# Performance work log

Measured on AMD Instinct MI355X. Metric: run time of the kernel, lower is better.

## Reference

```python
import jax, jax.numpy as jnp
import numpy as np

B, L, H, NH, NB = 8, 200, 128, 4, 2
HD = H // NH
ITEM_NUM, TIME_SPAN = 50000, 256
PAD = -2.0**32 + 1.0


def setup_inputs() -> dict:
    key = jax.random.key(0)
    ks = jax.random.split(key, 32)
    def g(i, shape, s=0.02):
        return jax.random.normal(ks[i], shape, jnp.float32) * s
    item_emb = g(0, (ITEM_NUM + 1, H)).at[0].set(0.0)  # padding_idx=0
    return dict(
        user_ids=jax.random.randint(ks[1], (B,), 0, 1000),
        log_seqs=jax.random.randint(ks[2], (B, L), 0, ITEM_NUM),
        time_matrices=jax.random.randint(ks[3], (B, L, L), 0, TIME_SPAN + 1),
        pos_seqs=jax.random.randint(ks[4], (B, L), 0, ITEM_NUM + 1),
        neg_seqs=jax.random.randint(ks[5], (B, L), 0, ITEM_NUM + 1),
        item_emb=item_emb,
        pos_K_emb=g(6, (L, H)), pos_V_emb=g(7, (L, H)),
        time_K_emb=g(8, (TIME_SPAN + 1, H)), time_V_emb=g(9, (TIME_SPAN + 1, H)),
        attn_ln_g=jnp.ones((NB, H)), attn_ln_b=jnp.zeros((NB, H)),
        Wq=g(10, (NB, H, H)), bq=jnp.zeros((NB, H)),
        Wk=g(11, (NB, H, H)), bk=jnp.zeros((NB, H)),
        Wv=g(12, (NB, H, H)), bv=jnp.zeros((NB, H)),
        fwd_ln_g=jnp.ones((NB, H)), fwd_ln_b=jnp.zeros((NB, H)),
        W1=g(13, (NB, H, H)), b1=jnp.zeros((NB, H)),
        W2=g(14, (NB, H, H)), b2=jnp.zeros((NB, H)),
        last_ln_g=jnp.ones((H,)), last_ln_b=jnp.zeros((H,)),
    )


def _ln(x, g, b, eps=1e-8):
    m = x.mean(-1, keepdims=True)
    v = jnp.var(x, axis=-1, keepdims=True)
    return (x - m) / jnp.sqrt(v + eps) * g + b


def _heads(x):
    # [..., H] -> [NH, ..., HD]; matches torch.cat(torch.split(x, HD, -1), 0)
    y = x.reshape(x.shape[:-1] + (NH, HD))
    return jnp.moveaxis(y, -2, 0)


def reference(user_ids, log_seqs, time_matrices, pos_seqs, neg_seqs, item_emb,
              pos_K_emb, pos_V_emb, time_K_emb, time_V_emb,
              attn_ln_g, attn_ln_b, Wq, bq, Wk, bk, Wv, bv,
              fwd_ln_g, fwd_ln_b, W1, b1, W2, b2, last_ln_g, last_ln_b):
    # user_ids is unused in the original forward as well.
    tmask = log_seqs == 0                                  # [B,L] True = pad
    keep = (~tmask)[..., None].astype(jnp.float32)
    seqs = item_emb[log_seqs] * np.float32(np.sqrt(H))
    seqs = seqs * keep
    pKh = _heads(pos_K_emb)                                # [NH,L,HD]
    pVh = _heads(pos_V_emb)
    tKh = _heads(time_K_emb[time_matrices])                # [NH,B,L,L,HD]
    tVh = _heads(time_V_emb[time_matrices])
    causal = ~jnp.tril(jnp.ones((L, L), bool))             # True above diag -> masked
    bad = tmask[:, :, None] | causal[None]                 # [B,L,L]
    scale = np.float32(np.sqrt(HD))
    for i in range(NB):
        Qin = _ln(seqs, attn_ln_g[i], attn_ln_b[i])
        Qh = _heads(Qin @ Wq[i].T + bq[i])                 # [NH,B,L,HD]
        Kh = _heads(seqs @ Wk[i].T + bk[i])
        Vh = _heads(seqs @ Wv[i].T + bv[i])
        attn = (jnp.einsum('nbqd,nbkd->nbqk', Qh, Kh)
                + jnp.einsum('nbqd,nkd->nbqk', Qh, pKh)
                + jnp.einsum('nbqkd,nbqd->nbqk', tKh, Qh)) / scale
        attn = jnp.where(bad[None], PAD, attn)
        attn = jax.nn.softmax(attn, axis=-1)
        out = (jnp.einsum('nbqk,nbkd->nbqd', attn, Vh)
               + jnp.einsum('nbqk,nkd->nbqd', attn, pVh)
               + jnp.einsum('nbqk,nbqkd->nbqd', attn, tVh))
        out = jnp.moveaxis(out, 0, -2).reshape(seqs.shape)  # merge heads -> [B,L,H]
        seqs = Qin + out                                    # residual uses LN'd Q (as in source)
        seqs = _ln(seqs, fwd_ln_g[i], fwd_ln_b[i])
        ff = jax.nn.relu(seqs @ W1[i].T + b1[i]) @ W2[i].T + b2[i] + seqs
        seqs = ff * keep
    log_feats = _ln(seqs, last_ln_g, last_ln_b)
    pos_logits = (log_feats * item_emb[pos_seqs]).sum(-1)   # [B,L]
    neg_logits = (log_feats * item_emb[neg_seqs]).sum(-1)
    return pos_logits, neg_logits
```

## Files before the change

kernel.cpp:

```cpp
#include <hip/hip_runtime.h>
#include <hip/hip_bf16.h>

#define BB 8
#define LL 200
#define HH 128
#define NHEAD 4
#define HDIM 32
#define NBLK 2
#define BL (BB * LL)
#define NT 257
#define QT 8
#define NQT 25
#define SSP 208
#define KTP 66
#define ASP 36
#define BSP 66
#define FASP 20
#define RSP 132

static constexpr float SQRT_H    = 11.313708498984761f;
static constexpr float INV_SCALE = 0.17677669529663687f;
static constexpr float PADV      = -4294967295.0f;

__global__ void k_qkv_gemm(const float* __restrict__ seqs_in,
                           const int* __restrict__ log_seqs,
                           const float* __restrict__ item_emb,
                           const float* __restrict__ g, const float* __restrict__ bia,
                           const float* __restrict__ Wq, const float* __restrict__ bq,
                           const float* __restrict__ Wk, const float* __restrict__ bk,
                           const float* __restrict__ Wv, const float* __restrict__ bv,
                           const float* __restrict__ posK, const float* __restrict__ posV,
                           float* __restrict__ Qin, float* __restrict__ Q,
                           float* __restrict__ K, float* __restrict__ V) {
    int mt = blockIdx.x / 6, nt = blockIdx.x % 6;
    int matsel = nt >> 1;
    int jb = (nt & 1) * 64;
    int row0 = mt * 32;
    int tid = threadIdx.x;
    __shared__ float As[128 * ASP];
    __shared__ float Bs[128 * BSP];

    {
        int r = tid >> 3, seg = tid & 7;
        int row = row0 + r;
        float4 vv[4];
        if (seqs_in) {
            #pragma unroll
            for (int i = 0; i < 4; i++)
                vv[i] = *(const float4*)(seqs_in + (size_t)row * HH + seg * 16 + i * 4);
        } else {
            int idx = log_seqs[row];
            if (idx == 0) {
                #pragma unroll
                for (int i = 0; i < 4; i++) vv[i] = make_float4(0.f, 0.f, 0.f, 0.f);
            } else {
                #pragma unroll
                for (int i = 0; i < 4; i++) {
                    float4 e = *(const float4*)(item_emb + (size_t)idx * HH + seg * 16 + i * 4);
                    vv[i] = make_float4(e.x * SQRT_H, e.y * SQRT_H, e.z * SQRT_H, e.w * SQRT_H);
                }
            }
        }
        if (matsel == 0) {
            float s = 0.f, s2 = 0.f;
            #pragma unroll
            for (int i = 0; i < 4; i++) {
                s  += vv[i].x + vv[i].y + vv[i].z + vv[i].w;
                s2 += vv[i].x * vv[i].x + vv[i].y * vv[i].y + vv[i].z * vv[i].z + vv[i].w * vv[i].w;
            }
            #pragma unroll
            for (int off = 1; off < 8; off <<= 1) {
                s  += __shfl_xor(s, off);
                s2 += __shfl_xor(s2, off);
            }
            float mean = s * (1.f / HH);
            float var  = s2 * (1.f / HH) - mean * mean;
            float inv  = 1.f / sqrtf(var + 1e-8f);
            #pragma unroll
            for (int i = 0; i < 4; i++) {
                int k = seg * 16 + i * 4;
                float4 g4 = *(const float4*)(g + k);
                float4 b4 = *(const float4*)(bia + k);
                float4 y;
                y.x = (vv[i].x - mean) * inv * g4.x + b4.x;
                y.y = (vv[i].y - mean) * inv * g4.y + b4.y;
                y.z = (vv[i].z - mean) * inv * g4.z + b4.z;
                y.w = (vv[i].w - mean) * inv * g4.w + b4.w;
                As[(k + 0) * ASP + r] = y.x;
                As[(k + 1) * ASP + r] = y.y;
                As[(k + 2) * ASP + r] = y.z;
                As[(k + 3) * ASP + r] = y.w;
                if (nt == 0) *(float4*)(Qin + (size_t)row * HH + k) = y;
            }
        } else {
            #pragma unroll
            for (int i = 0; i < 4; i++) {
                int k = seg * 16 + i * 4;
                As[(k + 0) * ASP + r] = vv[i].x;
                As[(k + 1) * ASP + r] = vv[i].y;
                As[(k + 2) * ASP + r] = vv[i].z;
                As[(k + 3) * ASP + r] = vv[i].w;
            }
        }
    }
    {
        const float* W = (matsel == 0) ? Wq : (matsel == 1) ? Wk : Wv;
        int k4 = tid & 31, jj0 = tid >> 5;
        #pragma unroll
        for (int p = 0; p < 8; p++) {
            int jj = jj0 + p * 8;
            float4 w = *(const float4*)(W + (size_t)(jb + jj) * HH + k4 * 4);
            Bs[(k4 * 4 + 0) * BSP + jj] = w.x;
            Bs[(k4 * 4 + 1) * BSP + jj] = w.y;
            Bs[(k4 * 4 + 2) * BSP + jj] = w.z;
            Bs[(k4 * 4 + 3) * BSP + jj] = w.w;
        }
    }
    __syncthreads();

    int my = tid >> 5, jx = tid & 31;
    float a00=0,a01=0,a10=0,a11=0,a20=0,a21=0,a30=0,a31=0;
    #pragma unroll 4
    for (int k = 0; k < HH; k++) {
        float4 a = *(const float4*)&As[k * ASP + my * 4];
        float2 b = *(const float2*)&Bs[k * BSP + jx * 2];
        a00 += a.x * b.x; a01 += a.x * b.y;
        a10 += a.y * b.x; a11 += a.y * b.y;
        a20 += a.z * b.x; a21 += a.z * b.y;
        a30 += a.w * b.x; a31 += a.w * b.y;
    }
    float accs[4][2] = {{a00,a01},{a10,a11},{a20,a21},{a30,a31}};
    int col = jb + jx * 2;
    if (matsel == 0) {
        float2 bb = *(const float2*)(bq + col);
        #pragma unroll
        for (int r = 0; r < 4; r++) {
            int row = row0 + my * 4 + r;
            float2 o = make_float2((accs[r][0] + bb.x) * INV_SCALE,
                                   (accs[r][1] + bb.y) * INV_SCALE);
            *(float2*)(Q + (size_t)row * HH + col) = o;
        }
    } else if (matsel == 1) {
        float2 bb = *(const float2*)(bk + col);
        #pragma unroll
        for (int r = 0; r < 4; r++) {
            int row = row0 + my * 4 + r;
            int l = row % LL;
            float2 pk = *(const float2*)(posK + (size_t)l * HH + col);
            float2 o = make_float2(accs[r][0] + bb.x + pk.x, accs[r][1] + bb.y + pk.y);
            *(float2*)(K + (size_t)row * HH + col) = o;
        }
    } else {
        float2 bb = *(const float2*)(bv + col);
        #pragma unroll
        for (int r = 0; r < 4; r++) {
            int row = row0 + my * 4 + r;
            int l = row % LL;
            float2 pv = *(const float2*)(posV + (size_t)l * HH + col);
            float2 o = make_float2(accs[r][0] + bb.x + pv.x, accs[r][1] + bb.y + pv.y);
            *(float2*)(V + (size_t)row * HH + col) = o;
        }
    }
}

__global__ void k_attn(const float* __restrict__ Q, const float* __restrict__ K,
                       const float* __restrict__ V,
                       const float* __restrict__ timeK, const float* __restrict__ timeV,
                       const int* __restrict__ tm,
                       float* __restrict__ att) {
    int bn = blockIdx.x & 31;
    int b = bn >> 2, n = bn & 3;
    int qt = (NQT - 1) - (blockIdx.x >> 5);
    int q0 = qt * QT;
    int kmax = q0 + QT - 1;
    int tid = threadIdx.x;
    int wv = tid >> 6, ln = tid & 63;

    __shared__ float Qs[QT * HDIM];
    __shared__ float KstT[HDIM * KTP];
    __shared__ float DTW[QT * NT];
    __shared__ float Ssc[QT * SSP];
    __shared__ int   tmst[QT * LL];
    __shared__ float Ost[QT * HDIM];

    Ost[tid] = 0.f;
    if (tid < 64) {
        int qi = tid >> 3, d4 = tid & 7;
        *(float4*)(Qs + qi * HDIM + d4 * 4) =
            *(const float4*)(Q + ((size_t)(b * LL + q0 + qi)) * HH + n * HDIM + d4 * 4);
    }
    #pragma unroll
    for (int qi = 0; qi < QT; qi++)
        if (tid < LL)
            tmst[qi * LL + tid] = tm[((size_t)(b * LL + q0 + qi)) * LL + tid];
    __syncthreads();

    int k2 = tid & 31, qi_c = tid >> 5;

    for (int c = 0; c < 5; c++) {
        #pragma unroll
        for (int p = 0; p < 2; p++) {
            int idx = tid + p * 256;
            int r = idx >> 3, d4 = idx & 7;
            int tau = c * 64 + r;
            float4 w = make_float4(0.f, 0.f, 0.f, 0.f);
            if (tau < NT) w = *(const float4*)(timeK + (size_t)tau * HH + n * HDIM + d4 * 4);
            KstT[(d4 * 4 + 0) * KTP + r] = w.x;
            KstT[(d4 * 4 + 1) * KTP + r] = w.y;
            KstT[(d4 * 4 + 2) * KTP + r] = w.z;
            KstT[(d4 * 4 + 3) * KTP + r] = w.w;
        }
        __syncthreads();
        float a0 = 0.f, a1 = 0.f;
        #pragma unroll 4
        for (int d = 0; d < HDIM; d++) {
            float qv = Qs[qi_c * HDIM + d];
            float2 kv = *(const float2*)&KstT[d * KTP + k2 * 2];
            a0 += qv * kv.x; a1 += qv * kv.y;
        }
        int tau0 = c * 64 + k2 * 2;
        if (tau0 < NT)     DTW[qi_c * NT + tau0]     = a0;
        if (tau0 + 1 < NT) DTW[qi_c * NT + tau0 + 1] = a1;
        __syncthreads();
    }

    int nch = (kmax >> 6) + 1;
    for (int c = 0; c < nch; c++) {
        #pragma unroll
        for (int p = 0; p < 2; p++) {
            int idx = tid + p * 256;
            int r = idx >> 3, d4 = idx & 7;
            int k = c * 64 + r;
            float4 w = make_float4(0.f, 0.f, 0.f, 0.f);
            if (k < LL) w = *(const float4*)(K + ((size_t)(b * LL + k)) * HH + n * HDIM + d4 * 4);
            KstT[(d4 * 4 + 0) * KTP + r] = w.x;
            KstT[(d4 * 4 + 1) * KTP + r] = w.y;
            KstT[(d4 * 4 + 2) * KTP + r] = w.z;
            KstT[(d4 * 4 + 3) * KTP + r] = w.w;
        }
        __syncthreads();
        float a0 = 0.f, a1 = 0.f;
        #pragma unroll 4
        for (int d = 0; d < HDIM; d++) {
            float qv = Qs[qi_c * HDIM + d];
            float2 kv = *(const float2*)&KstT[d * KTP + k2 * 2];
            a0 += qv * kv.x; a1 += qv * kv.y;
        }
        int q = q0 + qi_c;
        int k0 = c * 64 + k2 * 2;
        if (k0 <= kmax)
            Ssc[qi_c * SSP + k0] = (k0 <= q) ? (a0 + DTW[qi_c * NT + tmst[qi_c * LL + k0]]) : PADV;
        if (k0 + 1 <= kmax)
            Ssc[qi_c * SSP + k0 + 1] = (k0 + 1 <= q) ? (a1 + DTW[qi_c * NT + tmst[qi_c * LL + k0 + 1]]) : PADV;
        __syncthreads();
    }

    for (int idx = tid; idx < QT * NT; idx += 256) DTW[idx] = 0.f;
    __syncthreads();

    for (int rr = 0; rr < 2; rr++) {
        int qi = wv + rr * 4;
        int q = q0 + qi;
        float sv[4];
        float m = PADV;
        #pragma unroll
        for (int jj = 0; jj < 4; jj++) {
            int k = ln + 64 * jj;
            sv[jj] = (k <= q) ? Ssc[qi * SSP + k] : PADV;
            m = fmaxf(m, sv[jj]);
        }
        for (int off = 32; off; off >>= 1) m = fmaxf(m, __shfl_xor(m, off));
        float sum = 0.f;
        #pragma unroll
        for (int jj = 0; jj < 4; jj++) {
            int k = ln + 64 * jj;
            sv[jj] = (k <= q) ? __expf(sv[jj] - m) : 0.f;
            sum += sv[jj];
        }
        for (int off = 32; off; off >>= 1) sum += __shfl_xor(sum, off);
        float inv = 1.f / sum;
        #pragma unroll
        for (int jj = 0; jj < 4; jj++) {
            int k = ln + 64 * jj;
            float p = sv[jj] * inv;
            if (k < SSP) Ssc[qi * SSP + k] = (k <= q) ? p : 0.f;
            if (k <= q) atomicAdd(&DTW[qi * NT + tmst[qi * LL + k]], p);
        }
    }
    __syncthreads();

    int d = tid & 31, kg = tid >> 5;
    float acc[QT] = {0,0,0,0,0,0,0,0};
    const float* vb = V + ((size_t)(b * LL)) * HH + n * HDIM + d;
    for (int k = kg; k <= kmax; k += 8) {
        float v = vb[(size_t)k * HH];
        #pragma unroll
        for (int qi = 0; qi < QT; qi++) acc[qi] += Ssc[qi * SSP + k] * v;
    }
    const float* tvb = timeV + n * HDIM + d;
    for (int t = kg; t < NT; t += 8) {
        float v = tvb[(size_t)t * HH];
        #pragma unroll
        for (int qi = 0; qi < QT; qi++) acc[qi] += DTW[qi * NT + t] * v;
    }
    #pragma unroll
    for (int qi = 0; qi < QT; qi++) atomicAdd(&Ost[qi * HDIM + d], acc[qi]);
    __syncthreads();
    {
        int qi = tid >> 5;
        att[((size_t)(b * LL + q0 + qi)) * HH + n * HDIM + d] = Ost[qi * HDIM + d];
    }
}

__global__ void k_ff1(const float* __restrict__ Qin, const float* __restrict__ att,
                      const float* __restrict__ g, const float* __restrict__ bia,
                      const float* __restrict__ W1, const float* __restrict__ b1,
                      float* __restrict__ h1) {
    int mt = blockIdx.x >> 1, nt = blockIdx.x & 1;
    int jb = nt * 64;
    int row0 = mt * 16;
    int tid = threadIdx.x;
    __shared__ float As[128 * FASP];
    __shared__ float Bs[128 * BSP];

    {
        int r = tid >> 4, seg = tid & 15;
        int row = row0 + r;
        float4 vv[2];
        #pragma unroll
        for (int i = 0; i < 2; i++) {
            int k = seg * 8 + i * 4;
            float4 q4 = *(const float4*)(Qin + (size_t)row * HH + k);
            float4 a4 = *(const float4*)(att + (size_t)row * HH + k);
            vv[i] = make_float4(q4.x + a4.x, q4.y + a4.y, q4.z + a4.z, q4.w + a4.w);
        }
        float s = 0.f, s2 = 0.f;
        #pragma unroll
        for (int i = 0; i < 2; i++) {
            s  += vv[i].x + vv[i].y + vv[i].z + vv[i].w;
            s2 += vv[i].x * vv[i].x + vv[i].y * vv[i].y + vv[i].z * vv[i].z + vv[i].w * vv[i].w;
        }
        #pragma unroll
        for (int off = 1; off < 16; off <<= 1) {
            s  += __shfl_xor(s, off);
            s2 += __shfl_xor(s2, off);
        }
        float mean = s * (1.f / HH);
        float var  = s2 * (1.f / HH) - mean * mean;
        float inv  = 1.f / sqrtf(var + 1e-8f);
        #pragma unroll
        for (int i = 0; i < 2; i++) {
            int k = seg * 8 + i * 4;
            float4 g4 = *(const float4*)(g + k);
            float4 b4 = *(const float4*)(bia + k);
            As[(k + 0) * FASP + r] = (vv[i].x - mean) * inv * g4.x + b4.x;
            As[(k + 1) * FASP + r] = (vv[i].y - mean) * inv * g4.y + b4.y;
            As[(k + 2) * FASP + r] = (vv[i].z - mean) * inv * g4.z + b4.z;
            As[(k + 3) * FASP + r] = (vv[i].w - mean) * inv * g4.w + b4.w;
        }
    }
    {
        int k4 = tid & 31, jj0 = tid >> 5;
        #pragma unroll
        for (int p = 0; p < 8; p++) {
            int jj = jj0 + p * 8;
            float4 w = *(const float4*)(W1 + (size_t)(jb + jj) * HH + k4 * 4);
            Bs[(k4 * 4 + 0) * BSP + jj] = w.x;
            Bs[(k4 * 4 + 1) * BSP + jj] = w.y;
            Bs[(k4 * 4 + 2) * BSP + jj] = w.z;
            Bs[(k4 * 4 + 3) * BSP + jj] = w.w;
        }
    }
    __syncthreads();

    int my = tid >> 5, jx = tid & 31;
    float a00 = 0, a01 = 0, a10 = 0, a11 = 0;
    #pragma unroll 4
    for (int k = 0; k < HH; k++) {
        float2 a = *(const float2*)&As[k * FASP + my * 2];
        float2 b = *(const float2*)&Bs[k * BSP + jx * 2];
        a00 += a.x * b.x; a01 += a.x * b.y;
        a10 += a.y * b.x; a11 += a.y * b.y;
    }
    int col = jb + jx * 2;
    float2 bb = *(const float2*)(b1 + col);
    {
        int row = row0 + my * 2;
        float2 o0 = make_float2(fmaxf(a00 + bb.x, 0.f), fmaxf(a01 + bb.y, 0.f));
        float2 o1 = make_float2(fmaxf(a10 + bb.x, 0.f), fmaxf(a11 + bb.y, 0.f));
        *(float2*)(h1 + (size_t)row * HH + col) = o0;
        *(float2*)(h1 + (size_t)(row + 1) * HH + col) = o1;
    }
}

__global__ void k_ff2(const float* __restrict__ h1,
                      const float* __restrict__ Qin, const float* __restrict__ att,
                      const float* __restrict__ g, const float* __restrict__ bia,
                      const float* __restrict__ W2, const float* __restrict__ b2,
                      const int* __restrict__ log_seqs,
                      float* __restrict__ out) {
    int mt = blockIdx.x >> 1, nt = blockIdx.x & 1;
    int jb = nt * 64;
    int row0 = mt * 16;
    int tid = threadIdx.x;
    __shared__ float As[128 * FASP];
    __shared__ float Bs[128 * BSP];
    __shared__ float Rs[16 * RSP];
    __shared__ float mu[16], rstd[16];

    {
        int r = tid >> 4, seg = tid & 15;
        int row = row0 + r;
        #pragma unroll
        for (int i = 0; i < 2; i++) {
            int k = seg * 8 + i * 4;
            float4 h4 = *(const float4*)(h1 + (size_t)row * HH + k);
            As[(k + 0) * FASP + r] = h4.x;
            As[(k + 1) * FASP + r] = h4.y;
            As[(k + 2) * FASP + r] = h4.z;
            As[(k + 3) * FASP + r] = h4.w;
        }
        float s = 0.f, s2 = 0.f;
        #pragma unroll
        for (int i = 0; i < 2; i++) {
            int k = seg * 8 + i * 4;
            float4 q4 = *(const float4*)(Qin + (size_t)row * HH + k);
            float4 a4 = *(const float4*)(att + (size_t)row * HH + k);
            float4 v = make_float4(q4.x + a4.x, q4.y + a4.y, q4.z + a4.z, q4.w + a4.w);
            *(float4*)(Rs + r * RSP + k) = v;
            s  += v.x + v.y + v.z + v.w;
            s2 += v.x * v.x + v.y * v.y + v.z * v.z + v.w * v.w;
        }
        #pragma unroll
        for (int off = 1; off < 16; off <<= 1) {
            s  += __shfl_xor(s, off);
            s2 += __shfl_xor(s2, off);
        }
        float mean = s * (1.f / HH);
        float var  = s2 * (1.f / HH) - mean * mean;
        if (seg == 0) { mu[r] = mean; rstd[r] = 1.f / sqrtf(var + 1e-8f); }
    }
    {
        int k4 = tid & 31, jj0 = tid >> 5;
        #pragma unroll
        for (int p = 0; p < 8; p++) {
            int jj = jj0 + p * 8;
            float4 w = *(const float4*)(W2 + (size_t)(jb + jj) * HH + k4 * 4);
            Bs[(k4 * 4 + 0) * BSP + jj] = w.x;
            Bs[(k4 * 4 + 1) * BSP + jj] = w.y;
            Bs[(k4 * 4 + 2) * BSP + jj] = w.z;
            Bs[(k4 * 4 + 3) * BSP + jj] = w.w;
        }
    }
    __syncthreads();

    int my = tid >> 5, jx = tid & 31;
    float a00 = 0, a01 = 0, a10 = 0, a11 = 0;
    #pragma unroll 4
    for (int k = 0; k < HH; k++) {
        float2 a = *(const float2*)&As[k * FASP + my * 2];
        float2 b = *(const float2*)&Bs[k * BSP + jx * 2];
        a00 += a.x * b.x; a01 += a.x * b.y;
        a10 += a.y * b.x; a11 += a.y * b.y;
    }
    int col = jb + jx * 2;
    float2 bb = *(const float2*)(b2 + col);
    float2 g2 = *(const float2*)(g + col);
    float2 lb = *(const float2*)(bia + col);
    float accs[2][2] = {{a00, a01}, {a10, a11}};
    #pragma unroll
    for (int r = 0; r < 2; r++) {
        int ri = my * 2 + r;
        int row = row0 + ri;
        float m = mu[ri], iv = rstd[ri];
        float2 R = *(const float2*)&Rs[ri * RSP + col];
        float y0 = (R.x - m) * iv * g2.x + lb.x;
        float y1 = (R.y - m) * iv * g2.y + lb.y;
        float2 o = make_float2(accs[r][0] + bb.x + y0, accs[r][1] + bb.y + y1);
        if (log_seqs[row] == 0) o = make_float2(0.f, 0.f);
        *(float2*)(out + (size_t)row * HH + col) = o;
    }
}

__global__ void k_lnlogits(const float* __restrict__ seqs,
                           const float* __restrict__ g, const float* __restrict__ bia,
                           const float* __restrict__ item_emb,
                           const int* __restrict__ pos, const int* __restrict__ neg,
                           float* __restrict__ out) {
    int row = blockIdx.x;
    int h = threadIdx.x;
    float v = seqs[(size_t)row * HH + h];
    float s = v, s2 = v * v;
    for (int off = 32; off; off >>= 1) {
        s  += __shfl_xor(s, off);
        s2 += __shfl_xor(s2, off);
    }
    __shared__ float r1[2], r2[2];
    if ((h & 63) == 0) { r1[h >> 6] = s; r2[h >> 6] = s2; }
    __syncthreads();
    float mean = (r1[0] + r1[1]) * (1.f / HH);
    float var  = (r2[0] + r2[1]) * (1.f / HH) - mean * mean;
    float inv = 1.f / sqrtf(var + 1e-8f);
    float f = (v - mean) * inv * g[h] + bia[h];

    int ip = pos[row], in_ = neg[row];
    float vp = f * item_emb[(size_t)ip * HH + h];
    float vn = f * item_emb[(size_t)in_ * HH + h];
    for (int off = 32; off; off >>= 1) {
        vp += __shfl_xor(vp, off);
        vn += __shfl_xor(vn, off);
    }
    __shared__ float rp[2], rn[2];
    if ((h & 63) == 0) { rp[h >> 6] = vp; rn[h >> 6] = vn; }
    __syncthreads();
    if (h == 0) {
        out[row]      = rp[0] + rp[1];
        out[BL + row] = rn[0] + rn[1];
    }
}

extern "C" void kernel_launch(void* const* d_in, const int* in_sizes, int n_in,
                              void* d_out, int out_size, void* d_ws, size_t ws_size,
                              hipStream_t stream) {
    const int* log_seqs   = (const int*)d_in[1];
    const int* tm         = (const int*)d_in[2];
    const int* pos_seqs   = (const int*)d_in[3];
    const int* neg_seqs   = (const int*)d_in[4];
    const float* item_emb = (const float*)d_in[5];
    const float* posK     = (const float*)d_in[6];
    const float* posV     = (const float*)d_in[7];
    const float* timeK    = (const float*)d_in[8];
    const float* timeV    = (const float*)d_in[9];
    const float* attn_g   = (const float*)d_in[10];
    const float* attn_b   = (const float*)d_in[11];
    const float* Wq       = (const float*)d_in[12];
    const float* bq       = (const float*)d_in[13];
    const float* Wk       = (const float*)d_in[14];
    const float* bk       = (const float*)d_in[15];
    const float* Wv       = (const float*)d_in[16];
    const float* bv       = (const float*)d_in[17];
    const float* fwd_g    = (const float*)d_in[18];
    const float* fwd_b    = (const float*)d_in[19];
    const float* W1       = (const float*)d_in[20];
    const float* b1       = (const float*)d_in[21];
    const float* W2       = (const float*)d_in[22];
    const float* b2       = (const float*)d_in[23];
    const float* last_g   = (const float*)d_in[24];
    const float* last_b   = (const float*)d_in[25];

    float* seqs = (float*)d_ws;
    float* Qin  = seqs + (size_t)BL * HH;
    float* Qb   = Qin  + (size_t)BL * HH;
    float* Kb   = Qb   + (size_t)BL * HH;
    float* Vb   = Kb   + (size_t)BL * HH;
    float* att  = Vb   + (size_t)BL * HH;
    float* h1   = att  + (size_t)BL * HH;

    for (int i = 0; i < NBLK; i++) {
        k_qkv_gemm<<<300, 256, 0, stream>>>(i == 0 ? nullptr : seqs, log_seqs, item_emb,
                                            attn_g + i * HH, attn_b + i * HH,
                                            Wq + (size_t)i * HH * HH, bq + i * HH,
                                            Wk + (size_t)i * HH * HH, bk + i * HH,
                                            Wv + (size_t)i * HH * HH, bv + i * HH,
                                            posK, posV, Qin, Qb, Kb, Vb);
        k_attn<<<NQT * 32, 256, 0, stream>>>(Qb, Kb, Vb, timeK, timeV, tm, att);
        k_ff1<<<200, 256, 0, stream>>>(Qin, att, fwd_g + i * HH, fwd_b + i * HH,
                                       W1 + (size_t)i * HH * HH, b1 + i * HH, h1);
        k_ff2<<<200, 256, 0, stream>>>(h1, Qin, att, fwd_g + i * HH, fwd_b + i * HH,
                                       W2 + (size_t)i * HH * HH, b2 + i * HH,
                                       log_seqs, seqs);
    }
    k_lnlogits<<<BL, HH, 0, stream>>>(seqs, last_g, last_b, item_emb,
                                      pos_seqs, neg_seqs, (float*)d_out);
}
```

Baseline: 241.0 us.

## Shrink GEMM output tiles and use row-major LDS dot-product layout

The QKV, FF1 and FF2 GEMMs now use 16-column output tiles, giving four times more blocks so more CUs stay busy on this small problem. Shared-memory tiles become row-major with float4 stores, which removes the scalar transposed scatter stores, and each thread computes one or two outputs as vectorised dot products along K. FF2 now recomputes the residual from global memory instead of staging it in shared memory. In exchange, each thread reuses fewer registers, the LN prologue and weight loads repeat across more blocks, and row-major float4 reads may cause LDS bank conflicts.

```diff
diff --git a/kernel.cpp b/kernel.cpp
--- a/kernel.cpp
+++ b/kernel.cpp
@@ -13,10 +13,7 @@
 #define NQT 25
 #define SSP 208
 #define KTP 66
-#define ASP 36
-#define BSP 66
-#define FASP 20
-#define RSP 132
+#define TSP 132
 
 static constexpr float SQRT_H    = 11.313708498984761f;
 static constexpr float INV_SCALE = 0.17677669529663687f;
@@ -32,13 +29,13 @@
                            const float* __restrict__ posK, const float* __restrict__ posV,
                            float* __restrict__ Qin, float* __restrict__ Q,
                            float* __restrict__ K, float* __restrict__ V) {
-    int mt = blockIdx.x / 6, nt = blockIdx.x % 6;
-    int matsel = nt >> 1;
-    int jb = (nt & 1) * 64;
+    int mt = blockIdx.x / 24, nt = blockIdx.x % 24;
+    int matsel = nt >> 3;
+    int jb = (nt & 7) * 16;
     int row0 = mt * 32;
     int tid = threadIdx.x;
-    __shared__ float As[128 * ASP];
-    __shared__ float Bs[128 * BSP];
+    __shared__ float As[32 * TSP];
+    __shared__ float Bs[16 * TSP];
 
     {
         int r = tid >> 3, seg = tid & 7;
@@ -86,80 +83,55 @@
                 y.y = (vv[i].y - mean) * inv * g4.y + b4.y;
                 y.z = (vv[i].z - mean) * inv * g4.z + b4.z;
                 y.w = (vv[i].w - mean) * inv * g4.w + b4.w;
-                As[(k + 0) * ASP + r] = y.x;
-                As[(k + 1) * ASP + r] = y.y;
-                As[(k + 2) * ASP + r] = y.z;
-                As[(k + 3) * ASP + r] = y.w;
+                *(float4*)&As[r * TSP + k] = y;
                 if (nt == 0) *(float4*)(Qin + (size_t)row * HH + k) = y;
             }
         } else {
             #pragma unroll
-            for (int i = 0; i < 4; i++) {
-                int k = seg * 16 + i * 4;
-                As[(k + 0) * ASP + r] = vv[i].x;
-                As[(k + 1) * ASP + r] = vv[i].y;
-                As[(k + 2) * ASP + r] = vv[i].z;
-                As[(k + 3) * ASP + r] = vv[i].w;
-            }
+            for (int i = 0; i < 4; i++)
+                *(float4*)&As[r * TSP + seg * 16 + i * 4] = vv[i];
         }
     }
     {
         const float* W = (matsel == 0) ? Wq : (matsel == 1) ? Wk : Wv;
-        int k4 = tid & 31, jj0 = tid >> 5;
-        #pragma unroll
-        for (int p = 0; p < 8; p++) {
-            int jj = jj0 + p * 8;
-            float4 w = *(const float4*)(W + (size_t)(jb + jj) * HH + k4 * 4);
-            Bs[(k4 * 4 + 0) * BSP + jj] = w.x;
-            Bs[(k4 * 4 + 1) * BSP + jj] = w.y;
-            Bs[(k4 * 4 + 2) * BSP + jj] = w.z;
-            Bs[(k4 * 4 + 3) * BSP + jj] = w.w;
-        }
-    }
-    __syncthreads();
-
-    int my = tid >> 5, jx = tid & 31;
-    float a00=0,a01=0,a10=0,a11=0,a20=0,a21=0,a30=0,a31=0;
+        int j = tid >> 4, seg = tid & 15;
+        float4 w = *(const float4*)(W + (size_t)(jb + j) * HH + seg * 8);
+        float4 w2 = *(const float4*)(W + (size_t)(jb + j) * HH + seg * 8 + 4);
+        *(float4*)&Bs[j * TSP + seg * 8] = w;
+        *(float4*)&Bs[j * TSP + seg * 8 + 4] = w2;
+    }
+    __syncthreads();
+
+    int m = tid >> 3, jg = tid & 7;
+    float acc0 = 0.f, acc1 = 0.f;
+    const float* ar = &As[m * TSP];
+    const float* b0r = &Bs[(jg * 2) * TSP];
+    const float* b1r = &Bs[(jg * 2 + 1) * TSP];
     #pragma unroll 4
-    for (int k = 0; k < HH; k++) {
-        float4 a = *(const float4*)&As[k * ASP + my * 4];
-        float2 b = *(const float2*)&Bs[k * BSP + jx * 2];
-        a00 += a.x * b.x; a01 += a.x * b.y;
-        a10 += a.y * b.x; a11 += a.y * b.y;
-        a20 += a.z * b.x; a21 += a.z * b.y;
-        a30 += a.w * b.x; a31 += a.w * b.y;
-    }
-    float accs[4][2] = {{a00,a01},{a10,a11},{a20,a21},{a30,a31}};
-    int col = jb + jx * 2;
+    for (int k4 = 0; k4 < 32; k4++) {
+        float4 a = *(const float4*)(ar + k4 * 4);
+        float4 b0 = *(const float4*)(b0r + k4 * 4);
+        float4 b1 = *(const float4*)(b1r + k4 * 4);
+        acc0 += a.x * b0.x + a.y * b0.y + a.z * b0.z + a.w * b0.w;
+        acc1 += a.x * b1.x + a.y * b1.y + a.z * b1.z + a.w * b1.w;
+    }
+    int row = row0 + m;
+    int col = jb + jg * 2;
+    int l = row % LL;
     if (matsel == 0) {
         float2 bb = *(const float2*)(bq + col);
-        #pragma unroll
-        for (int r = 0; r < 4; r++) {
-            int row = row0 + my * 4 + r;
-            float2 o = make_float2((accs[r][0] + bb.x) * INV_SCALE,
-                                   (accs[r][1] + bb.y) * INV_SCALE);
-            *(float2*)(Q + (size_t)row * HH + col) = o;
-        }
+        *(float2*)(Q + (size_t)row * HH + col) =
+            make_float2((acc0 + bb.x) * INV_SCALE, (acc1 + bb.y) * INV_SCALE);
     } else if (matsel == 1) {
         float2 bb = *(const float2*)(bk + col);
-        #pragma unroll
-        for (int r = 0; r < 4; r++) {
-            int row = row0 + my * 4 + r;
-            int l = row % LL;
-            float2 pk = *(const float2*)(posK + (size_t)l * HH + col);
-            float2 o = make_float2(accs[r][0] + bb.x + pk.x, accs[r][1] + bb.y + pk.y);
-            *(float2*)(K + (size_t)row * HH + col) = o;
-        }
+        float2 pk = *(const float2*)(posK + (size_t)l * HH + col);
+        *(float2*)(K + (size_t)row * HH + col) =
+            make_float2(acc0 + bb.x + pk.x, acc1 + bb.y + pk.y);
     } else {
         float2 bb = *(const float2*)(bv + col);
-        #pragma unroll
-        for (int r = 0; r < 4; r++) {
-            int row = row0 + my * 4 + r;
-            int l = row % LL;
-            float2 pv = *(const float2*)(posV + (size_t)l * HH + col);
-            float2 o = make_float2(accs[r][0] + bb.x + pv.x, accs[r][1] + bb.y + pv.y);
-            *(float2*)(V + (size_t)row * HH + col) = o;
-        }
+        float2 pv = *(const float2*)(posV + (size_t)l * HH + col);
+        *(float2*)(V + (size_t)row * HH + col) =
+            make_float2(acc0 + bb.x + pv.x, acc1 + bb.y + pv.y);
     }
 }
 
@@ -308,7 +280,7 @@
     __syncthreads();
     {
         int qi = tid >> 5;
-        att[((size_t)(b * LL + q0 + qi)) * HH + n * HDIM + d] = Ost[qi * HDIM + d];
+        att[((size_t)(b * LL + q0 + qi)) * HH + n * HDIM + (tid & 31)] = Ost[tid];
     }
 }
 
@@ -316,12 +288,11 @@
                       const float* __restrict__ g, const float* __restrict__ bia,
                       const float* __restrict__ W1, const float* __restrict__ b1,
                       float* __restrict__ h1) {
-    int mt = blockIdx.x >> 1, nt = blockIdx.x & 1;
-    int jb = nt * 64;
+    int mt = blockIdx.x >> 3, jb = (blockIdx.x & 7) * 16;
     int row0 = mt * 16;
     int tid = threadIdx.x;
-    __shared__ float As[128 * FASP];
-    __shared__ float Bs[128 * BSP];
+    __shared__ float As[16 * TSP];
+    __shared__ float Bs[16 * TSP];
 
     {
         int r = tid >> 4, seg = tid & 15;
@@ -353,44 +324,34 @@
             int k = seg * 8 + i * 4;
             float4 g4 = *(const float4*)(g + k);
             float4 b4 = *(const float4*)(bia + k);
-            As[(k + 0) * FASP + r] = (vv[i].x - mean) * inv * g4.x + b4.x;
-            As[(k + 1) * FASP + r] = (vv[i].y - mean) * inv * g4.y + b4.y;
-            As[(k + 2) * FASP + r] = (vv[i].z - mean) * inv * g4.z + b4.z;
-            As[(k + 3) * FASP + r] = (vv[i].w - mean) * inv * g4.w + b4.w;
-        }
-    }
-    {
-        int k4 = tid & 31, jj0 = tid >> 5;
-        #pragma unroll
-        for (int p = 0; p < 8; p++) {
-            int jj = jj0 + p * 8;
-            float4 w = *(const float4*)(W1 + (size_t)(jb + jj) * HH + k4 * 4);
-            Bs[(k4 * 4 + 0) * BSP + jj] = w.x;
-            Bs[(k4 * 4 + 1) * BSP + jj] = w.y;
-            Bs[(k4 * 4 + 2) * BSP + jj] = w.z;
-            Bs[(k4 * 4 + 3) * BSP + jj] = w.w;
-        }
-    }
-    __syncthreads();
-
-    int my = tid >> 5, jx = tid & 31;
-    float a00 = 0, a01 = 0, a10 = 0, a11 = 0;
+            float4 y;
+            y.x = (vv[i].x - mean) * inv * g4.x + b4.x;
+            y.y = (vv[i].y - mean) * inv * g4.y + b4.y;
+            y.z = (vv[i].z - mean) * inv * g4.z + b4.z;
+            y.w = (vv[i].w - mean) * inv * g4.w + b4.w;
+            *(float4*)&As[r * TSP + k] = y;
+        }
+    }
+    {
+        int j = tid >> 4, seg = tid & 15;
+        *(float4*)&Bs[j * TSP + seg * 8]     = *(const float4*)(W1 + (size_t)(jb + j) * HH + seg * 8);
+        *(float4*)&Bs[j * TSP + seg * 8 + 4] = *(const float4*)(W1 + (size_t)(jb + j) * HH + seg * 8 + 4);
+    }
+    __syncthreads();
+
+    int m = tid >> 4, j = tid & 15;
+    float acc = 0.f;
+    const float* ar = &As[m * TSP];
+    const float* br = &Bs[j * TSP];
     #pragma unroll 4
-    for (int k = 0; k < HH; k++) {
-        float2 a = *(const float2*)&As[k * FASP + my * 2];
-        float2 b = *(const float2*)&Bs[k * BSP + jx * 2];
-        a00 += a.x * b.x; a01 += a.x * b.y;
-        a10 += a.y * b.x; a11 += a.y * b.y;
-    }
-    int col = jb + jx * 2;
-    float2 bb = *(const float2*)(b1 + col);
-    {
-        int row = row0 + my * 2;
-        float2 o0 = make_float2(fmaxf(a00 + bb.x, 0.f), fmaxf(a01 + bb.y, 0.f));
-        float2 o1 = make_float2(fmaxf(a10 + bb.x, 0.f), fmaxf(a11 + bb.y, 0.f));
-        *(float2*)(h1 + (size_t)row * HH + col) = o0;
-        *(float2*)(h1 + (size_t)(row + 1) * HH + col) = o1;
-    }
+    for (int k4 = 0; k4 < 32; k4++) {
+        float4 a = *(const float4*)(ar + k4 * 4);
+        float4 b = *(const float4*)(br + k4 * 4);
+        acc += a.x * b.x + a.y * b.y + a.z * b.z + a.w * b.w;
+    }
+    int col = jb + j;
+    float t = acc + b1[col];
+    h1[(size_t)(row0 + m) * HH + col] = t > 0.f ? t : 0.f;
 }
 
 __global__ void k_ff2(const float* __restrict__ h1,
@@ -399,13 +360,11 @@
                       const float* __restrict__ W2, const float* __restrict__ b2,
                       const int* __restrict__ log_seqs,
                       float* __restrict__ out) {
-    int mt = blockIdx.x >> 1, nt = blockIdx.x & 1;
-    int jb = nt * 64;
+    int mt = blockIdx.x >> 3, jb = (blockIdx.x & 7) * 16;
     int row0 = mt * 16;
     int tid = threadIdx.x;
-    __shared__ float As[128 * FASP];
-    __shared__ float Bs[128 * BSP];
-    __shared__ float Rs[16 * RSP];
+    __shared__ float As[16 * TSP];
+    __shared__ float Bs[16 * TSP];
     __shared__ float mu[16], rstd[16];
 
     {
@@ -414,11 +373,7 @@
         #pragma unroll
         for (int i = 0; i < 2; i++) {
             int k = seg * 8 + i * 4;
-            float4 h4 = *(const float4*)(h1 + (size_t)row * HH + k);
-            As[(k + 0) * FASP + r] = h4.x;
-            As[(k + 1) * FASP + r] = h4.y;
-            As[(k + 2) * FASP + r] = h4.z;
-            As[(k + 3) * FASP + r] = h4.w;
+            *(float4*)&As[r * TSP + k] = *(const float4*)(h1 + (size_t)row * HH + k);
         }
         float s = 0.f, s2 = 0.f;
         #pragma unroll
@@ -427,7 +382,6 @@
             float4 q4 = *(const float4*)(Qin + (size_t)row * HH + k);
             float4 a4 = *(const float4*)(att + (size_t)row * HH + k);
             float4 v = make_float4(q4.x + a4.x, q4.y + a4.y, q4.z + a4.z, q4.w + a4.w);
-            *(float4*)(Rs + r * RSP + k) = v;
             s  += v.x + v.y + v.z + v.w;
             s2 += v.x * v.x + v.y * v.y + v.z * v.z + v.w * v.w;
         }
@@ -441,45 +395,29 @@
         if (seg == 0) { mu[r] = mean; rstd[r] = 1.f / sqrtf(var + 1e-8f); }
     }
     {
-        int k4 = tid & 31, jj0 = tid >> 5;
-        #pragma unroll
-        for (int p = 0; p < 8; p++) {
-            int jj = jj0 + p * 8;
-            float4 w = *(const float4*)(W2 + (size_t)(jb + jj) * HH + k4 * 4);
-            Bs[(k4 * 4 + 0) * BSP + jj] = w.x;
-            Bs[(k4 * 4 + 1) * BSP + jj] = w.y;
-            Bs[(k4 * 4 + 2) * BSP + jj] = w.z;
-            Bs[(k4 * 4 + 3) * BSP + jj] = w.w;
-        }
-    }
-    __syncthreads();
-
-    int my = tid >> 5, jx = tid & 31;
-    float a00 = 0, a01 = 0, a10 = 0, a11 = 0;
+        int j = tid >> 4, seg = tid & 15;
+        *(float4*)&Bs[j * TSP + seg * 8]     = *(const float4*)(W2 + (size_t)(jb + j) * HH + seg * 8);
+        *(float4*)&Bs[j * TSP + seg * 8 + 4] = *(const float4*)(W2 + (size_t)(jb + j) * HH + seg * 8 + 4);
+    }
+    __syncthreads();
+
+    int m = tid >> 4, j = tid & 15;
+    float acc = 0.f;
+    const float* ar = &As[m * TSP];
+    const float* br = &Bs[j * TSP];
     #pragma unroll 4
-    for (int k = 0; k < HH; k++) {
-        float2 a = *(const float2*)&As[k * FASP + my * 2];
-        float2 b = *(const float2*)&Bs[k * BSP + jx * 2];
-        a00 += a.x * b.x; a01 += a.x * b.y;
-        a10 += a.y * b.x; a11 += a.y * b.y;
-    }
-    int col = jb + jx * 2;
-    float2 bb = *(const float2*)(b2 + col);
-    float2 g2 = *(const float2*)(g + col);
-    float2 lb = *(const float2*)(bia + col);
-    float accs[2][2] = {{a00, a01}, {a10, a11}};
-    #pragma unroll
-    for (int r = 0; r < 2; r++) {
-        int ri = my * 2 + r;
-        int row = row0 + ri;
-        float m = mu[ri], iv = rstd[ri];
-        float2 R = *(const float2*)&Rs[ri * RSP + col];
-        float y0 = (R.x - m) * iv * g2.x + lb.x;
-        float y1 = (R.y - m) * iv * g2.y + lb.y;
-        float2 o = make_float2(accs[r][0] + bb.x + y0, accs[r][1] + bb.y + y1);
-        if (log_seqs[row] == 0) o = make_float2(0.f, 0.f);
-        *(float2*)(out + (size_t)row * HH + col) = o;
-    }
+    for (int k4 = 0; k4 < 32; k4++) {
+        float4 a = *(const float4*)(ar + k4 * 4);
+        float4 b = *(const float4*)(br + k4 * 4);
+        acc += a.x * b.x + a.y * b.y + a.z * b.z + a.w * b.w;
+    }
+    int row = row0 + m;
+    int col = jb + j;
+    float resid = Qin[(size_t)row * HH + col] + att[(size_t)row * HH + col];
+    float y = (resid - mu[m]) * rstd[m] * g[col] + bia[col];
+    float o = acc + b2[col] + y;
+    if (log_seqs[row] == 0) o = 0.f;
+    out[(size_t)row * HH + col] = o;
 }
 
 __global__ void k_lnlogits(const float* __restrict__ seqs,
@@ -557,16 +495,16 @@
     float* h1   = att  + (size_t)BL * HH;
 
     for (int i = 0; i < NBLK; i++) {
-        k_qkv_gemm<<<300, 256, 0, stream>>>(i == 0 ? nullptr : seqs, log_seqs, item_emb,
-                                            attn_g + i * HH, attn_b + i * HH,
-                                            Wq + (size_t)i * HH * HH, bq + i * HH,
-                                            Wk + (size_t)i * HH * HH, bk + i * HH,
-                                            Wv + (size_t)i * HH * HH, bv + i * HH,
-                                            posK, posV, Qin, Qb, Kb, Vb);
+        k_qkv_gemm<<<1200, 256, 0, stream>>>(i == 0 ? nullptr : seqs, log_seqs, item_emb,
+                                             attn_g + i * HH, attn_b + i * HH,
+                                             Wq + (size_t)i * HH * HH, bq + i * HH,
+                                             Wk + (size_t)i * HH * HH, bk + i * HH,
+                                             Wv + (size_t)i * HH * HH, bv + i * HH,
+                                             posK, posV, Qin, Qb, Kb, Vb);
         k_attn<<<NQT * 32, 256, 0, stream>>>(Qb, Kb, Vb, timeK, timeV, tm, att);
-        k_ff1<<<200, 256, 0, stream>>>(Qin, att, fwd_g + i * HH, fwd_b + i * HH,
+        k_ff1<<<800, 256, 0, stream>>>(Qin, att, fwd_g + i * HH, fwd_b + i * HH,
                                        W1 + (size_t)i * HH * HH, b1 + i * HH, h1);
-        k_ff2<<<200, 256, 0, stream>>>(h1, Qin, att, fwd_g + i * HH, fwd_b + i * HH,
+        k_ff2<<<800, 256, 0, stream>>>(h1, Qin, att, fwd_g + i * HH, fwd_b + i * HH,
                                        W2 + (size_t)i * HH * HH, b2 + i * HH,
                                        log_seqs, seqs);
     }
```

After: 238.4 us. No clear change (-1.1%).
